# Kernel tuning notes

Hardware: AMD Instinct MI355X
Metric: run time of the kernel (lower is better)

Reference implementation:

```python
import jax, jax.numpy as jnp
import numpy as np

B, N = 4, 1024
D_MODEL, N_HEADS, D_HEAD, D_COORD = 512, 8, 64, 2


def setup_inputs() -> dict:
    key = jax.random.key(0)
    ks = jax.random.split(key, 8)
    sd = 1.0 / np.sqrt(D_MODEL)
    return {
        "x": jax.random.normal(ks[0], (B, N, D_MODEL), dtype=jnp.float32),
        "positions": jax.random.uniform(ks[1], (N, D_COORD), dtype=jnp.float32) * 32.0,
        "W_Q": jax.random.normal(ks[2], (D_MODEL, N_HEADS * D_HEAD), dtype=jnp.float32) * sd,
        "W_K": jax.random.normal(ks[3], (D_MODEL, N_HEADS * D_HEAD), dtype=jnp.float32) * sd,
        "W_V": jax.random.normal(ks[4], (D_MODEL, N_HEADS * D_HEAD), dtype=jnp.float32) * sd,
        "W_O": jax.random.normal(ks[5], (N_HEADS * D_HEAD, D_MODEL), dtype=jnp.float32) * sd,
        "U": jax.random.normal(ks[6], (N_HEADS, D_HEAD, D_HEAD), dtype=jnp.float32),
        "freqs": jax.random.normal(ks[7], (N_HEADS, D_HEAD // 2, D_COORD), dtype=jnp.float32),
    }


def reference(x, positions, W_Q, W_K, W_V, W_O, U, freqs):
    # x: (B,N,d_model); positions: (N,d_coord); U: (H,dh,dh); freqs: (H,m,d_coord)
    Bn, Nn, _ = x.shape
    H, dh, _ = U.shape
    m = dh // 2
    scale = (dh // 2) ** -0.5

    Q = (x @ W_Q).reshape(Bn, Nn, H, dh)
    K = (x @ W_K).reshape(Bn, Nn, H, dh)
    V = (x @ W_V).reshape(Bn, Nn, H, dh)

    # Active-subspace projector: Pi = qr(U)[0] @ qr(U)[0].T per head
    Uq = jax.vmap(lambda u: jnp.linalg.qr(u)[0])(U)              # (H,dh,dh)
    P = jnp.einsum('hde,hfe->hdf', Uq, Uq)                       # U U^T
    Qp = jnp.einsum('bnhd,hdf->bhnf', Q, P)                      # (B,H,N,dh)
    Kp = jnp.einsum('bnhd,hdf->bhnf', K, P)

    # Relative rotation: R_rel(r_j - r_i) is block-diag 2x2 rotations with
    # angle theta_ijm = freqs_m . (r_j - r_i) = a_jm - a_im (separable), so
    # q^T R(r_j-r_i) k = (R(a_i)q)^T (R(a_j)k)  -- exact RoPE identity.
    ang = jnp.einsum('nc,hmc->hnm', positions, freqs)            # (H,N,m)
    c = jnp.cos(ang)[None]                                       # (1,H,N,m)
    s = jnp.sin(ang)[None]

    def rot(v):  # v: (B,H,N,dh) -> rotated (even, odd) halves (B,H,N,m)
        ve, vo = v[..., ::2], v[..., 1::2]
        return ve * c - vo * s, ve * s + vo * c

    qe, qo = rot(Qp)
    ke, ko = rot(Kp)
    scores = (jnp.einsum('bhim,bhjm->bhij', qe, ke)
              + jnp.einsum('bhim,bhjm->bhij', qo, ko)) * scale   # (B,H,N,N)
    w = jax.nn.softmax(scores, axis=-1)
    out = jnp.einsum('bhij,bjhd->bihd', w, V).reshape(Bn, Nn, H * dh)
    return out @ W_O
```

## Files before the change

kernel.cpp:

```cpp
#include <hip/hip_runtime.h>
#include <hip/hip_bf16.h>
#include <math.h>

#define NBATCH 4
#define NSEQ   1024
#define DMODEL 512
#define NH     8
#define DH     64
#define MROWS  (NBATCH*NSEQ)
#define MHALF  (DH/2)

typedef __attribute__((ext_vector_type(8))) short bf16x8;
typedef __attribute__((ext_vector_type(4))) float floatx4;

__device__ __forceinline__ uint f2bf2(float lo, float hi) {
    union { __hip_bfloat162 h; uint u; } v;
    v.h = __float22bfloat162_rn(make_float2(lo, hi));
    return v.u;
}

__global__ __launch_bounds__(256) void prep_kernel(
    const float* __restrict__ pos, const float* __restrict__ freqs,
    const float* __restrict__ x,
    const float* __restrict__ Wq, const float* __restrict__ Wk,
    const float* __restrict__ Wv, const float* __restrict__ Wo,
    float* __restrict__ cosT, float* __restrict__ sinT,
    ushort* __restrict__ xb, ushort* __restrict__ Wt)
{
    __shared__ float T[64][65];
    const int bid = blockIdx.x;
    const int tid = threadIdx.x;

    if (bid < 1024) {
        int idx = bid * 256 + tid;
        int m = idx & 31;
        int n = (idx >> 5) & 1023;
        int h = idx >> 15;
        float a = pos[n*2+0] * freqs[(h*MHALF+m)*2+0]
                + pos[n*2+1] * freqs[(h*MHALF+m)*2+1];
        cosT[idx] = cosf(a);
        sinT[idx] = sinf(a);
    } else if (bid < 2048) {
        int idx = ((bid - 1024) * 256 + tid) * 8;
        float4 a = *(const float4*)&x[idx];
        float4 b = *(const float4*)&x[idx+4];
        uint4 pk;
        pk.x = f2bf2(a.x, a.y);
        pk.y = f2bf2(a.z, a.w);
        pk.z = f2bf2(b.x, b.y);
        pk.w = f2bf2(b.z, b.w);
        *(uint4*)&xb[idx] = pk;
    } else {
        int b2 = bid - 2048;
        int n0g = (b2 & 31) * 64;
        int k0  = (b2 >> 5) * 64;
        int mat = n0g >> 9;
        const float* W = (mat == 0) ? Wq : ((mat == 1) ? Wk : ((mat == 2) ? Wv : Wo));
        int n0 = n0g & 511;
        int c = tid & 63, r = tid >> 6;
        #pragma unroll
        for (int i = 0; i < 16; i++)
            T[r + i*4][c] = W[(k0 + r + i*4) * DMODEL + n0 + c];
        __syncthreads();
        int nl = tid >> 2;
        int kg = tid & 3;
        #pragma unroll
        for (int g = 0; g < 4; g++) {
            int kl = kg * 16 + g * 4;
            uint2 pk;
            pk.x = f2bf2(T[kl+0][nl], T[kl+1][nl]);
            pk.y = f2bf2(T[kl+2][nl], T[kl+3][nl]);
            *(uint2*)&Wt[(size_t)(n0g + nl) * DMODEL + k0 + kl] = pk;
        }
    }
}

__global__ __launch_bounds__(256) void qkv_gemm(
    const ushort* __restrict__ xb, const ushort* __restrict__ Wt,
    const float* __restrict__ cosT, const float* __restrict__ sinT,
    ushort* __restrict__ Qb, ushort* __restrict__ Kb, ushort* __restrict__ Vt)
{
    __shared__ __align__(16) ushort S[16896];
    ushort* As = S;
    ushort* Bs = S + 64*72;
    float (*Cs)[132] = (float(*)[132])S;

    const int cb = blockIdx.x;
    const int rb = blockIdx.y;
    const int mat = cb >> 2;
    const int c0 = (cb & 3) * 128;
    const int r0 = rb * 64;
    const int ng0 = mat * 512 + c0;

    const int tid = threadIdx.x;
    const int w = tid >> 6, l = tid & 63;
    const int lr = l & 15, lg = l >> 4;
    const int wr = w & 1;
    const int wc = w >> 1;

    const int arow = tid >> 2;
    const int acol = (tid & 3) * 16;
    const int brow = tid >> 1;
    const int bcol = (tid & 1) * 32;

    floatx4 acc[2][4];
    #pragma unroll
    for (int mi = 0; mi < 2; mi++)
        #pragma unroll
        for (int nt = 0; nt < 4; nt++) acc[mi][nt] = (floatx4){0.f,0.f,0.f,0.f};

    const ushort* pa = &xb[(size_t)(r0 + arow) * DMODEL + acol];
    const ushort* pb = &Wt[(size_t)(ng0 + brow) * DMODEL + bcol];
    uint4 ra0 = *(const uint4*)pa;
    uint4 ra1 = *(const uint4*)(pa + 8);
    uint4 rb0 = *(const uint4*)pb;
    uint4 rb1 = *(const uint4*)(pb + 8);
    uint4 rb2 = *(const uint4*)(pb + 16);
    uint4 rb3 = *(const uint4*)(pb + 24);

    for (int k0 = 0; k0 < DMODEL; k0 += 64) {
        __syncthreads();
        *(uint4*)&As[arow*72 + acol]     = ra0;
        *(uint4*)&As[arow*72 + acol + 8] = ra1;
        *(uint4*)&Bs[brow*72 + bcol]      = rb0;
        *(uint4*)&Bs[brow*72 + bcol + 8]  = rb1;
        *(uint4*)&Bs[brow*72 + bcol + 16] = rb2;
        *(uint4*)&Bs[brow*72 + bcol + 24] = rb3;
        __syncthreads();

        if (k0 + 64 < DMODEL) {
            const ushort* na = &xb[(size_t)(r0 + arow) * DMODEL + k0 + 64 + acol];
            const ushort* nb = &Wt[(size_t)(ng0 + brow) * DMODEL + k0 + 64 + bcol];
            ra0 = *(const uint4*)na;
            ra1 = *(const uint4*)(na + 8);
            rb0 = *(const uint4*)nb;
            rb1 = *(const uint4*)(nb + 8);
            rb2 = *(const uint4*)(nb + 16);
            rb3 = *(const uint4*)(nb + 24);
        }

        #pragma unroll
        for (int ks = 0; ks < 2; ks++) {
            bf16x8 af0 = *(const bf16x8*)&As[(wr*32 +  0 + lr)*72 + ks*32 + lg*8];
            bf16x8 af1 = *(const bf16x8*)&As[(wr*32 + 16 + lr)*72 + ks*32 + lg*8];
            #pragma unroll
            for (int nt = 0; nt < 4; nt++) {
                bf16x8 bf = *(const bf16x8*)&Bs[(wc*64 + nt*16 + lr)*72 + ks*32 + lg*8];
                acc[0][nt] = __builtin_amdgcn_mfma_f32_16x16x32_bf16(af0, bf, acc[0][nt], 0, 0, 0);
                acc[1][nt] = __builtin_amdgcn_mfma_f32_16x16x32_bf16(af1, bf, acc[1][nt], 0, 0, 0);
            }
        }
    }

    __syncthreads();
    #pragma unroll
    for (int mi = 0; mi < 2; mi++)
        #pragma unroll
        for (int nt = 0; nt < 4; nt++)
            #pragma unroll
            for (int r = 0; r < 4; r++)
                Cs[wr*32 + mi*16 + lg*4 + r][wc*64 + nt*16 + lr] = acc[mi][nt][r];
    __syncthreads();

    const int tx = tid & 31, ty = tid >> 5;
    const int dloc = tx * 4;
    const int head = (c0 + dloc) >> 6;
    const int dh = (c0 + dloc) & 63;

    if (mat == 2) {
        int rowbase = r0 + ty * 8;
        int b = rowbase >> 10, n0 = rowbase & 1023;
        #pragma unroll
        for (int j = 0; j < 4; j++) {
            size_t base = ((size_t)(b * NH + head) * DH + dh + j) * NSEQ + n0;
            uint2 p1, p2;
            p1.x = f2bf2(Cs[ty*8 + 0][dloc + j], Cs[ty*8 + 1][dloc + j]);
            p1.y = f2bf2(Cs[ty*8 + 2][dloc + j], Cs[ty*8 + 3][dloc + j]);
            p2.x = f2bf2(Cs[ty*8 + 4][dloc + j], Cs[ty*8 + 5][dloc + j]);
            p2.y = f2bf2(Cs[ty*8 + 6][dloc + j], Cs[ty*8 + 7][dloc + j]);
            *(uint2*)&Vt[base]     = p1;
            *(uint2*)&Vt[base + 4] = p2;
        }
    } else {
        ushort* dst = (mat == 0) ? Qb : Kb;
        const float qs2 = (mat == 0) ? (0.17677669529663687f * 1.4426950408889634f) : 1.0f;
        #pragma unroll
        for (int i = 0; i < 8; i++) {
            int row = r0 + ty * 8 + i;
            int b = row >> 10, n = row & 1023;
            float v[4];
            #pragma unroll
            for (int p = 0; p < 2; p++) {
                int m = (dh >> 1) + p;
                float c = cosT[(head * NSEQ + n) * MHALF + m] * qs2;
                float s = sinT[(head * NSEQ + n) * MHALF + m] * qs2;
                float ve = Cs[ty*8 + i][dloc + 2*p];
                float vo = Cs[ty*8 + i][dloc + 2*p + 1];
                v[2*p]     = ve * c - vo * s;
                v[2*p + 1] = ve * s + vo * c;
            }
            uint2 pk;
            pk.x = f2bf2(v[0], v[1]);
            pk.y = f2bf2(v[2], v[3]);
            *(uint2*)&dst[((size_t)(b * NH + head) * NSEQ + n) * DH + dh] = pk;
        }
    }
}

__global__ __launch_bounds__(256, 4) void attn_kernel(
    const ushort* __restrict__ Qb, const ushort* __restrict__ Kb,
    const ushort* __restrict__ Vt, ushort* __restrict__ Obb)
{
    __shared__ __align__(16) ushort S[2*64*72 + 32*72];
    ushort* Ks = S;
    ushort* Vs = S + 64*72;
    ushort* Ps = S + 2*64*72;

    const int tid = threadIdx.x;
    const int w = tid >> 6, l = tid & 63;
    const int lr = l & 15, lg = l >> 4;
    const int qs = w & 1;
    const int jh = w >> 1;
    const int bh = blockIdx.y, q0 = blockIdx.x * 32;

    const ushort* Qg = Qb + (size_t)bh * NSEQ * DH;
    const ushort* Kg = Kb + (size_t)bh * NSEQ * DH;
    const ushort* Vg = Vt + (size_t)bh * DH * NSEQ;

    bf16x8 qf[2];
    #pragma unroll
    for (int ks = 0; ks < 2; ks++)
        qf[ks] = *(const bf16x8*)(Qg + (size_t)(q0 + 16*qs + lr) * DH + ks*32 + lg*8);

    floatx4 ot[4];
    #pragma unroll
    for (int i = 0; i < 4; i++) ot[i] = (floatx4){0.f, 0.f, 0.f, 0.f};
    float l_lane = 0.f;

    const int sr = tid >> 2;
    const int sc = (tid & 3) * 16;

    const ushort* kp = Kg + (size_t)sr * DH + sc;
    uint4 ka  = *(const uint4*)kp;
    uint4 kb2 = *(const uint4*)(kp + 8);
    const ushort* vp = Vg + (size_t)sr * NSEQ + sc;
    uint4 va  = *(const uint4*)vp;
    uint4 vb2 = *(const uint4*)(vp + 8);

    for (int jt = 0; jt < 16; jt++) {
        __syncthreads();
        *(uint4*)&Ks[sr*72 + sc]     = ka;
        *(uint4*)&Ks[sr*72 + sc + 8] = kb2;
        *(uint4*)&Vs[sr*72 + sc]     = va;
        *(uint4*)&Vs[sr*72 + sc + 8] = vb2;
        __syncthreads();

        if (jt < 15) {
            const ushort* kn = Kg + (size_t)((jt+1)*64 + sr) * DH + sc;
            ka  = *(const uint4*)kn;
            kb2 = *(const uint4*)(kn + 8);
            const ushort* vn = Vg + (size_t)sr * NSEQ + (jt+1)*64 + sc;
            va  = *(const uint4*)vn;
            vb2 = *(const uint4*)(vn + 8);
        }

        #pragma unroll
        for (int jm2 = 0; jm2 < 2; jm2++) {
            const int jm = jh*2 + jm2;
            floatx4 acc = (floatx4){0.f, 0.f, 0.f, 0.f};
            #pragma unroll
            for (int ks = 0; ks < 2; ks++) {
                bf16x8 af = *(const bf16x8*)&Ks[(jm*16 + lr)*72 + ks*32 + lg*8];
                acc = __builtin_amdgcn_mfma_f32_16x16x32_bf16(af, qf[ks], acc, 0, 0, 0);
            }
            float p0 = __builtin_amdgcn_exp2f(acc[0]);
            float p1 = __builtin_amdgcn_exp2f(acc[1]);
            float p2 = __builtin_amdgcn_exp2f(acc[2]);
            float p3 = __builtin_amdgcn_exp2f(acc[3]);
            l_lane += (p0 + p1) + (p2 + p3);
            uint2 pk;
            pk.x = f2bf2(p0, p1);
            pk.y = f2bf2(p2, p3);
            *(uint2*)&Ps[(16*qs + lr)*72 + jm*16 + lg*4] = pk;
        }

        {
            bf16x8 pf = *(const bf16x8*)&Ps[(16*qs + lr)*72 + jh*32 + lg*8];
            #pragma unroll
            for (int dt = 0; dt < 4; dt++) {
                bf16x8 af = *(const bf16x8*)&Vs[(dt*16 + lr)*72 + jh*32 + lg*8];
                ot[dt] = __builtin_amdgcn_mfma_f32_16x16x32_bf16(af, pf, ot[dt], 0, 0, 0);
            }
        }
    }

    l_lane += __shfl_xor(l_lane, 16, 64);
    l_lane += __shfl_xor(l_lane, 32, 64);

    __syncthreads();
    float* Os = (float*)S;
    float* Ls = (float*)(S + 5120);
    if (w >= 2) {
        #pragma unroll
        for (int dt = 0; dt < 4; dt++)
            *(float4*)&Os[(qs*64 + l)*20 + dt*4] = *(float4*)&ot[dt];
        if (lg == 0) Ls[qs*16 + lr] = l_lane;
    }
    __syncthreads();
    if (w < 2) {
        float lsum = l_lane + Ls[qs*16 + lr];
        float inv = 1.f / lsum;
        int n = q0 + 16*qs + lr;
        size_t obase = ((size_t)bh * NSEQ + n) * DH;
        #pragma unroll
        for (int dt = 0; dt < 4; dt++) {
            float4 p = *(const float4*)&Os[(qs*64 + l)*20 + dt*4];
            uint2 pk;
            pk.x = f2bf2((ot[dt][0] + p.x) * inv, (ot[dt][1] + p.y) * inv);
            pk.y = f2bf2((ot[dt][2] + p.z) * inv, (ot[dt][3] + p.w) * inv);
            *(uint2*)&Obb[obase + dt*16 + lg*4] = pk;
        }
    }
}

__global__ __launch_bounds__(256) void out_gemm(
    const ushort* __restrict__ Obb, const ushort* __restrict__ Wt,
    float* __restrict__ out)
{
    __shared__ __align__(16) ushort AB[2 * 64 * 72];
    ushort* As = AB;
    ushort* Bs = AB + 64 * 72;
    float (*Cs)[65] = (float(*)[65])AB;

    const int cb = blockIdx.x;
    const int rb = blockIdx.y;
    const int c0 = cb * 64, r0 = rb * 64;

    const int tid = threadIdx.x;
    const int w = tid >> 6, l = tid & 63;
    const int lr = l & 15, lg = l >> 4;
    const int srow = tid >> 2;
    const int scol = (tid & 3) * 16;

    const int arow = r0 + srow;
    const int b = arow >> 10, n = arow & 1023;

    floatx4 acc[4];
    #pragma unroll
    for (int nt = 0; nt < 4; nt++) acc[nt] = (floatx4){0.f,0.f,0.f,0.f};

    #define A_ADDR(K0) (&Obb[((size_t)(b*NH + ((K0) >> 6)) * NSEQ + n) * DH + scol])

    const ushort* pb0 = &Wt[(size_t)(1536 + c0 + srow) * DMODEL + scol];
    uint4 ra0 = *(const uint4*)A_ADDR(0);
    uint4 ra1 = *(const uint4*)(A_ADDR(0) + 8);
    uint4 rb0 = *(const uint4*)pb0;
    uint4 rb1 = *(const uint4*)(pb0 + 8);

    for (int k0 = 0; k0 < DMODEL; k0 += 64) {
        __syncthreads();
        *(uint4*)&As[srow*72 + scol]     = ra0;
        *(uint4*)&As[srow*72 + scol + 8] = ra1;
        *(uint4*)&Bs[srow*72 + scol]     = rb0;
        *(uint4*)&Bs[srow*72 + scol + 8] = rb1;
        __syncthreads();

        if (k0 + 64 < DMODEL) {
            const ushort* na = A_ADDR(k0 + 64);
            const ushort* nb = &Wt[(size_t)(1536 + c0 + srow) * DMODEL + (k0 + 64) + scol];
            ra0 = *(const uint4*)na;
            ra1 = *(const uint4*)(na + 8);
            rb0 = *(const uint4*)nb;
            rb1 = *(const uint4*)(nb + 8);
        }

        #pragma unroll
        for (int ks = 0; ks < 2; ks++) {
            bf16x8 af = *(const bf16x8*)&As[(16*w + lr)*72 + ks*32 + lg*8];
            #pragma unroll
            for (int nt = 0; nt < 4; nt++) {
                bf16x8 bf = *(const bf16x8*)&Bs[(nt*16 + lr)*72 + ks*32 + lg*8];
                acc[nt] = __builtin_amdgcn_mfma_f32_16x16x32_bf16(af, bf, acc[nt], 0, 0, 0);
            }
        }
    }
    #undef A_ADDR

    __syncthreads();
    #pragma unroll
    for (int nt = 0; nt < 4; nt++)
        #pragma unroll
        for (int r = 0; r < 4; r++)
            Cs[16*w + lg*4 + r][nt*16 + lr] = acc[nt][r];
    __syncthreads();

    const int tx = tid & 15, ty = tid >> 4;
    #pragma unroll
    for (int i = 0; i < 4; i++) {
        float4 o;
        o.x = Cs[ty*4 + i][tx*4 + 0];
        o.y = Cs[ty*4 + i][tx*4 + 1];
        o.z = Cs[ty*4 + i][tx*4 + 2];
        o.w = Cs[ty*4 + i][tx*4 + 3];
        *(float4*)&out[(size_t)(r0 + ty*4 + i) * DMODEL + c0 + tx*4] = o;
    }
}

extern "C" void kernel_launch(void* const* d_in, const int* in_sizes, int n_in,
                              void* d_out, int out_size, void* d_ws, size_t ws_size,
                              hipStream_t stream) {
    const float* x         = (const float*)d_in[0];
    const float* positions = (const float*)d_in[1];
    const float* Wq        = (const float*)d_in[2];
    const float* Wk        = (const float*)d_in[3];
    const float* Wv        = (const float*)d_in[4];
    const float* Wo        = (const float*)d_in[5];
    const float* freqs     = (const float*)d_in[7];
    float* out = (float*)d_out;

    float*  ws    = (float*)d_ws;
    float*  cosT  = ws;
    float*  sinT  = cosT + NH*NSEQ*MHALF;
    ushort* xb    = (ushort*)(sinT + NH*NSEQ*MHALF);
    ushort* Wt    = xb + (size_t)MROWS*DMODEL;
    ushort* Qb    = Wt + (size_t)2048*DMODEL;
    ushort* Kb    = Qb + (size_t)NBATCH*NH*NSEQ*DH;
    ushort* Vt    = Kb + (size_t)NBATCH*NH*NSEQ*DH;
    ushort* Obb   = Vt + (size_t)NBATCH*NH*NSEQ*DH;

    prep_kernel<<<dim3(2304), 256, 0, stream>>>(positions, freqs, x, Wq, Wk, Wv, Wo,
                                                cosT, sinT, xb, Wt);
    qkv_gemm<<<dim3(12, 64), 256, 0, stream>>>(xb, Wt, cosT, sinT, Qb, Kb, Vt);
    attn_kernel<<<dim3(32, 32), 256, 0, stream>>>(Qb, Kb, Vt, Obb);
    out_gemm<<<dim3(8, 64), 256, 0, stream>>>(Obb, Wt, out);
}
```

Before: 120.8 us.

## Split attention keys across waves with direct global K/V fragment loads

The attention kernel now gives each wave a disjoint quarter of the key sequence for all 32 queries. K and V fragments are loaded straight from global memory into registers instead of being staged through shared memory, which removes the per-tile __syncthreads barriers. P is staged in a per-wave LDS region, and the partial outputs and row sums of the four waves are combined in shared memory at the end. The cost is more register pressure, unshared global loads with no explicit prefetch or overlap, and a larger cross-wave reduction.

```diff
diff --git a/kernel.cpp b/kernel.cpp
--- a/kernel.cpp
+++ b/kernel.cpp
@@ -211,115 +211,146 @@
     const ushort* __restrict__ Qb, const ushort* __restrict__ Kb,
     const ushort* __restrict__ Vt, ushort* __restrict__ Obb)
 {
-    __shared__ __align__(16) ushort S[2*64*72 + 32*72];
-    ushort* Ks = S;
-    ushort* Vs = S + 64*72;
-    ushort* Ps = S + 2*64*72;
+    __shared__ __align__(16) ushort S[17664];
 
     const int tid = threadIdx.x;
     const int w = tid >> 6, l = tid & 63;
     const int lr = l & 15, lg = l >> 4;
-    const int qs = w & 1;
-    const int jh = w >> 1;
     const int bh = blockIdx.y, q0 = blockIdx.x * 32;
 
     const ushort* Qg = Qb + (size_t)bh * NSEQ * DH;
     const ushort* Kg = Kb + (size_t)bh * NSEQ * DH;
     const ushort* Vg = Vt + (size_t)bh * DH * NSEQ;
 
-    bf16x8 qf[2];
-    #pragma unroll
-    for (int ks = 0; ks < 2; ks++)
-        qf[ks] = *(const bf16x8*)(Qg + (size_t)(q0 + 16*qs + lr) * DH + ks*32 + lg*8);
-
-    floatx4 ot[4];
-    #pragma unroll
-    for (int i = 0; i < 4; i++) ot[i] = (floatx4){0.f, 0.f, 0.f, 0.f};
-    float l_lane = 0.f;
-
-    const int sr = tid >> 2;
-    const int sc = (tid & 3) * 16;
-
-    const ushort* kp = Kg + (size_t)sr * DH + sc;
-    uint4 ka  = *(const uint4*)kp;
-    uint4 kb2 = *(const uint4*)(kp + 8);
-    const ushort* vp = Vg + (size_t)sr * NSEQ + sc;
-    uint4 va  = *(const uint4*)vp;
-    uint4 vb2 = *(const uint4*)(vp + 8);
-
-    for (int jt = 0; jt < 16; jt++) {
-        __syncthreads();
-        *(uint4*)&Ks[sr*72 + sc]     = ka;
-        *(uint4*)&Ks[sr*72 + sc + 8] = kb2;
-        *(uint4*)&Vs[sr*72 + sc]     = va;
-        *(uint4*)&Vs[sr*72 + sc + 8] = vb2;
-        __syncthreads();
-
-        if (jt < 15) {
-            const ushort* kn = Kg + (size_t)((jt+1)*64 + sr) * DH + sc;
-            ka  = *(const uint4*)kn;
-            kb2 = *(const uint4*)(kn + 8);
-            const ushort* vn = Vg + (size_t)sr * NSEQ + (jt+1)*64 + sc;
-            va  = *(const uint4*)vn;
-            vb2 = *(const uint4*)(vn + 8);
-        }
-
-        #pragma unroll
-        for (int jm2 = 0; jm2 < 2; jm2++) {
-            const int jm = jh*2 + jm2;
-            floatx4 acc = (floatx4){0.f, 0.f, 0.f, 0.f};
-            #pragma unroll
-            for (int ks = 0; ks < 2; ks++) {
-                bf16x8 af = *(const bf16x8*)&Ks[(jm*16 + lr)*72 + ks*32 + lg*8];
-                acc = __builtin_amdgcn_mfma_f32_16x16x32_bf16(af, qf[ks], acc, 0, 0, 0);
-            }
-            float p0 = __builtin_amdgcn_exp2f(acc[0]);
-            float p1 = __builtin_amdgcn_exp2f(acc[1]);
-            float p2 = __builtin_amdgcn_exp2f(acc[2]);
-            float p3 = __builtin_amdgcn_exp2f(acc[3]);
-            l_lane += (p0 + p1) + (p2 + p3);
-            uint2 pk;
-            pk.x = f2bf2(p0, p1);
-            pk.y = f2bf2(p2, p3);
-            *(uint2*)&Ps[(16*qs + lr)*72 + jm*16 + lg*4] = pk;
-        }
+    ushort* Ps = S + w * 1280;
+
+    bf16x8 qf00 = *(const bf16x8*)(Qg + (size_t)(q0 +  0 + lr) * DH +  0 + lg*8);
+    bf16x8 qf01 = *(const bf16x8*)(Qg + (size_t)(q0 +  0 + lr) * DH + 32 + lg*8);
+    bf16x8 qf10 = *(const bf16x8*)(Qg + (size_t)(q0 + 16 + lr) * DH +  0 + lg*8);
+    bf16x8 qf11 = *(const bf16x8*)(Qg + (size_t)(q0 + 16 + lr) * DH + 32 + lg*8);
+
+    floatx4 ot00 = (floatx4){0.f,0.f,0.f,0.f}, ot01 = ot00, ot02 = ot00, ot03 = ot00;
+    floatx4 ot10 = ot00, ot11 = ot00, ot12 = ot00, ot13 = ot00;
+    float l0 = 0.f, l1 = 0.f;
+
+    const int j0base = w * 256;
+
+    for (int t = 0; t < 8; t++) {
+        const int j0 = j0base + t * 32;
+
+        const ushort* kp = Kg + (size_t)(j0 + lr) * DH + lg*8;
+        bf16x8 k00 = *(const bf16x8*)(kp);
+        bf16x8 k01 = *(const bf16x8*)(kp + 32);
+        bf16x8 k10 = *(const bf16x8*)(kp + 16*DH);
+        bf16x8 k11 = *(const bf16x8*)(kp + 16*DH + 32);
+
+        floatx4 a00 = (floatx4){0.f,0.f,0.f,0.f}, a01 = a00, a10 = a00, a11 = a00;
+        a00 = __builtin_amdgcn_mfma_f32_16x16x32_bf16(k00, qf00, a00, 0, 0, 0);
+        a00 = __builtin_amdgcn_mfma_f32_16x16x32_bf16(k01, qf01, a00, 0, 0, 0);
+        a01 = __builtin_amdgcn_mfma_f32_16x16x32_bf16(k00, qf10, a01, 0, 0, 0);
+        a01 = __builtin_amdgcn_mfma_f32_16x16x32_bf16(k01, qf11, a01, 0, 0, 0);
+        a10 = __builtin_amdgcn_mfma_f32_16x16x32_bf16(k10, qf00, a10, 0, 0, 0);
+        a10 = __builtin_amdgcn_mfma_f32_16x16x32_bf16(k11, qf01, a10, 0, 0, 0);
+        a11 = __builtin_amdgcn_mfma_f32_16x16x32_bf16(k10, qf10, a11, 0, 0, 0);
+        a11 = __builtin_amdgcn_mfma_f32_16x16x32_bf16(k11, qf11, a11, 0, 0, 0);
+
+        const ushort* vp = Vg + (size_t)lr * NSEQ + j0 + lg*8;
+        bf16x8 v0 = *(const bf16x8*)(vp);
+        bf16x8 v1 = *(const bf16x8*)(vp + 16*NSEQ);
+        bf16x8 v2 = *(const bf16x8*)(vp + 32*NSEQ);
+        bf16x8 v3 = *(const bf16x8*)(vp + 48*NSEQ);
 
         {
-            bf16x8 pf = *(const bf16x8*)&Ps[(16*qs + lr)*72 + jh*32 + lg*8];
-            #pragma unroll
-            for (int dt = 0; dt < 4; dt++) {
-                bf16x8 af = *(const bf16x8*)&Vs[(dt*16 + lr)*72 + jh*32 + lg*8];
-                ot[dt] = __builtin_amdgcn_mfma_f32_16x16x32_bf16(af, pf, ot[dt], 0, 0, 0);
-            }
-        }
-    }
-
-    l_lane += __shfl_xor(l_lane, 16, 64);
-    l_lane += __shfl_xor(l_lane, 32, 64);
+            float p0 = __builtin_amdgcn_exp2f(a00[0]);
+            float p1 = __builtin_amdgcn_exp2f(a00[1]);
+            float p2 = __builtin_amdgcn_exp2f(a00[2]);
+            float p3 = __builtin_amdgcn_exp2f(a00[3]);
+            l0 += (p0 + p1) + (p2 + p3);
+            uint2 pk; pk.x = f2bf2(p0, p1); pk.y = f2bf2(p2, p3);
+            *(uint2*)&Ps[lr*40 + 0 + lg*4] = pk;
+        }
+        {
+            float p0 = __builtin_amdgcn_exp2f(a10[0]);
+            float p1 = __builtin_amdgcn_exp2f(a10[1]);
+            float p2 = __builtin_amdgcn_exp2f(a10[2]);
+            float p3 = __builtin_amdgcn_exp2f(a10[3]);
+            l0 += (p0 + p1) + (p2 + p3);
+            uint2 pk; pk.x = f2bf2(p0, p1); pk.y = f2bf2(p2, p3);
+            *(uint2*)&Ps[lr*40 + 16 + lg*4] = pk;
+        }
+        {
+            float p0 = __builtin_amdgcn_exp2f(a01[0]);
+            float p1 = __builtin_amdgcn_exp2f(a01[1]);
+            float p2 = __builtin_amdgcn_exp2f(a01[2]);
+            float p3 = __builtin_amdgcn_exp2f(a01[3]);
+            l1 += (p0 + p1) + (p2 + p3);
+            uint2 pk; pk.x = f2bf2(p0, p1); pk.y = f2bf2(p2, p3);
+            *(uint2*)&Ps[(16 + lr)*40 + 0 + lg*4] = pk;
+        }
+        {
+            float p0 = __builtin_amdgcn_exp2f(a11[0]);
+            float p1 = __builtin_amdgcn_exp2f(a11[1]);
+            float p2 = __builtin_amdgcn_exp2f(a11[2]);
+            float p3 = __builtin_amdgcn_exp2f(a11[3]);
+            l1 += (p0 + p1) + (p2 + p3);
+            uint2 pk; pk.x = f2bf2(p0, p1); pk.y = f2bf2(p2, p3);
+            *(uint2*)&Ps[(16 + lr)*40 + 16 + lg*4] = pk;
+        }
+
+        bf16x8 pf0 = *(const bf16x8*)&Ps[( 0 + lr)*40 + lg*8];
+        bf16x8 pf1 = *(const bf16x8*)&Ps[(16 + lr)*40 + lg*8];
+
+        ot00 = __builtin_amdgcn_mfma_f32_16x16x32_bf16(v0, pf0, ot00, 0, 0, 0);
+        ot01 = __builtin_amdgcn_mfma_f32_16x16x32_bf16(v1, pf0, ot01, 0, 0, 0);
+        ot02 = __builtin_amdgcn_mfma_f32_16x16x32_bf16(v2, pf0, ot02, 0, 0, 0);
+        ot03 = __builtin_amdgcn_mfma_f32_16x16x32_bf16(v3, pf0, ot03, 0, 0, 0);
+        ot10 = __builtin_amdgcn_mfma_f32_16x16x32_bf16(v0, pf1, ot10, 0, 0, 0);
+        ot11 = __builtin_amdgcn_mfma_f32_16x16x32_bf16(v1, pf1, ot11, 0, 0, 0);
+        ot12 = __builtin_amdgcn_mfma_f32_16x16x32_bf16(v2, pf1, ot12, 0, 0, 0);
+        ot13 = __builtin_amdgcn_mfma_f32_16x16x32_bf16(v3, pf1, ot13, 0, 0, 0);
+    }
+
+    l0 += __shfl_xor(l0, 16, 64);
+    l0 += __shfl_xor(l0, 32, 64);
+    l1 += __shfl_xor(l1, 16, 64);
+    l1 += __shfl_xor(l1, 32, 64);
 
     __syncthreads();
     float* Os = (float*)S;
-    float* Ls = (float*)(S + 5120);
-    if (w >= 2) {
-        #pragma unroll
-        for (int dt = 0; dt < 4; dt++)
-            *(float4*)&Os[(qs*64 + l)*20 + dt*4] = *(float4*)&ot[dt];
-        if (lg == 0) Ls[qs*16 + lr] = l_lane;
-    }
-    __syncthreads();
-    if (w < 2) {
-        float lsum = l_lane + Ls[qs*16 + lr];
+    float* Ls = (float*)(S + 17408);
+    {
+        const int r0o = (w*32 + lr)*68;
+        *(float4*)&Os[r0o + 0*16 + lg*4]  = *(float4*)&ot00;
+        *(float4*)&Os[r0o + 1*16 + lg*4]  = *(float4*)&ot01;
+        *(float4*)&Os[r0o + 2*16 + lg*4]  = *(float4*)&ot02;
+        *(float4*)&Os[r0o + 3*16 + lg*4]  = *(float4*)&ot03;
+        const int r1o = (w*32 + 16 + lr)*68;
+        *(float4*)&Os[r1o + 0*16 + lg*4]  = *(float4*)&ot10;
+        *(float4*)&Os[r1o + 1*16 + lg*4]  = *(float4*)&ot11;
+        *(float4*)&Os[r1o + 2*16 + lg*4]  = *(float4*)&ot12;
+        *(float4*)&Os[r1o + 3*16 + lg*4]  = *(float4*)&ot13;
+        if (lg == 0) { Ls[w*32 + lr] = l0; Ls[w*32 + 16 + lr] = l1; }
+    }
+    __syncthreads();
+    {
+        const int q  = tid >> 3;
+        const int d8 = (tid & 7) * 8;
+        float lsum = Ls[q] + Ls[32 + q] + Ls[64 + q] + Ls[96 + q];
         float inv = 1.f / lsum;
-        int n = q0 + 16*qs + lr;
-        size_t obase = ((size_t)bh * NSEQ + n) * DH;
-        #pragma unroll
-        for (int dt = 0; dt < 4; dt++) {
-            float4 p = *(const float4*)&Os[(qs*64 + l)*20 + dt*4];
-            uint2 pk;
-            pk.x = f2bf2((ot[dt][0] + p.x) * inv, (ot[dt][1] + p.y) * inv);
-            pk.y = f2bf2((ot[dt][2] + p.z) * inv, (ot[dt][3] + p.w) * inv);
-            *(uint2*)&Obb[obase + dt*16 + lg*4] = pk;
-        }
+        float4 s0 = {0.f,0.f,0.f,0.f}, s1 = {0.f,0.f,0.f,0.f};
+        #pragma unroll
+        for (int wv = 0; wv < 4; wv++) {
+            float4 u0 = *(const float4*)&Os[(wv*32 + q)*68 + d8];
+            float4 u1 = *(const float4*)&Os[(wv*32 + q)*68 + d8 + 4];
+            s0.x += u0.x; s0.y += u0.y; s0.z += u0.z; s0.w += u0.w;
+            s1.x += u1.x; s1.y += u1.y; s1.z += u1.z; s1.w += u1.w;
+        }
+        uint4 pk;
+        pk.x = f2bf2(s0.x * inv, s0.y * inv);
+        pk.y = f2bf2(s0.z * inv, s0.w * inv);
+        pk.z = f2bf2(s1.x * inv, s1.y * inv);
+        pk.w = f2bf2(s1.z * inv, s1.w * inv);
+        *(uint4*)&Obb[((size_t)bh * NSEQ + q0 + q) * DH + d8] = pk;
     }
 }
 
```

Measured after the change: 132.3 us. 9.5% more time.
